# Performance work log

Hardware: AMD Instinct MI355X
Metric: run time of the kernel (lower is better)

Reference implementation:

```python
import jax, jax.numpy as jnp
import numpy as np

N_NODES = 50000
EPS = 1e-7      # GENConv message epsilon
BN_EPS = 1e-5   # BatchNorm1d eps
N_AGGR = 2


def setup_inputs() -> dict:
    key = jax.random.key(0)
    ks = jax.random.split(key, 8)
    C = 64
    E = 800000
    x = jax.random.normal(ks[0], (N_NODES, C), dtype=jnp.float32)
    edge_index = jax.random.randint(ks[1], (2, E), 0, N_NODES, dtype=jnp.int64)
    # per-GENConv MLP params, stacked over the N_AGGR layers
    W1 = jax.random.normal(ks[2], (N_AGGR, C, 2 * C), dtype=jnp.float32) * (1.0 / np.sqrt(C))
    b1 = jnp.zeros((N_AGGR, 2 * C), dtype=jnp.float32)
    gamma = jnp.ones((N_AGGR, 2 * C), dtype=jnp.float32)
    beta = jnp.zeros((N_AGGR, 2 * C), dtype=jnp.float32)
    W2 = jax.random.normal(ks[3], (N_AGGR, 2 * C, C), dtype=jnp.float32) * (1.0 / np.sqrt(2 * C))
    b2 = jnp.zeros((N_AGGR, C), dtype=jnp.float32)
    t = jnp.ones((N_AGGR,), dtype=jnp.float32)  # learnable softmax temperature
    return {"x": x, "edge_index": edge_index, "W1": W1, "b1": b1,
            "gamma": gamma, "beta": beta, "W2": W2, "b2": b2, "t": t}


def _gen_conv(x, src, dst, W1_l, b1_l, gamma_l, beta_l, W2_l, b2_l, t_l):
    # message: relu(x_j) + eps  (edge_attr is None)
    m = jax.nn.relu(x[src]) + EPS                      # [E, C]
    # softmax aggregation over edges grouped by destination node
    logits = m * t_l                                   # [E, C]
    seg_max = jax.ops.segment_max(logits, dst, num_segments=N_NODES)  # [N, C]
    ex = jnp.exp(logits - seg_max[dst])                # [E, C]
    den = jax.ops.segment_sum(ex, dst, num_segments=N_NODES)          # [N, C]
    alpha = ex / (den[dst] + 1e-16)                    # [E, C]
    aggr = jax.ops.segment_sum(m * alpha, dst, num_segments=N_NODES)  # [N, C]
    # residual then MLP: Linear(C,2C) -> BatchNorm1d (train-mode stats) -> ReLU -> Linear(2C,C)
    h = aggr + x
    h = h @ W1_l + b1_l                                # [N, 2C]
    mean = h.mean(axis=0)
    var = h.var(axis=0)                                # biased variance (torch BN)
    h = (h - mean) / jnp.sqrt(var + BN_EPS) * gamma_l + beta_l
    h = jax.nn.relu(h)
    h = h @ W2_l + b2_l                                # [N, C]
    return h


def reference(x, edge_index, W1, b1, gamma, beta, W2, b2, t):
    src = edge_index[0]
    dst = edge_index[1]
    for l in range(N_AGGR):
        x = _gen_conv(x, src, dst, W1[l], b1[l], gamma[l], beta[l], W2[l], b2[l], t[l])
        x = jax.nn.relu(x)
        # dropout in eval mode == identity
    return x
```

## Files before the change

### kernel.cpp

```cpp
#include <hip/hip_runtime.h>
#include <math.h>

#define NN 50000
#define EPSM 1e-7f
#define BN_EPS 1e-5f
#define NBK 391


__global__ __launch_bounds__(256) void bucket_hist_kernel(
    const int* __restrict__ dst, int* __restrict__ bhist, int E,
    unsigned* __restrict__ mm0, float* __restrict__ bn0){
  __shared__ int h[NBK];
  int t = threadIdx.x;
  if (blockIdx.x == 0){
    if (t < 64) mm0[t] = 0x7F7FFFFFu;
    else if (t < 128) mm0[t] = 0u;
    bn0[t] = 0.f;
  }
  for (int i = t; i < NBK; i += 256) h[i] = 0;
  __syncthreads();
  int e0 = blockIdx.x * 4096;
  int cnt = min(4096, E - e0);
  for (int i = t; i < cnt; i += 256) atomicAdd(&h[dst[e0 + i] >> 7], 1);
  __syncthreads();
  for (int i = t; i < NBK; i += 256) if (h[i]) atomicAdd(&bhist[i], h[i]);
}

__global__ void bucket_scan_kernel(const int* __restrict__ bhist,
                                   int* __restrict__ bbase, int* __restrict__ gcur){
  int lane = threadIdx.x;
  int loc[7]; int s = 0;
#pragma unroll
  for (int k = 0; k < 7; ++k){
    int i = lane * 7 + k;
    int v = (i < NBK) ? bhist[i] : 0;
    loc[k] = s; s += v;
  }
  int sc = s;
#pragma unroll
  for (int o = 1; o < 64; o <<= 1){
    int n = __shfl_up(sc, o);
    if (lane >= o) sc += n;
  }
  int exc = sc - s;
#pragma unroll
  for (int k = 0; k < 7; ++k){
    int i = lane * 7 + k;
    if (i < NBK){ bbase[i] = exc + loc[k]; gcur[i] = exc + loc[k]; }
    else if (i == NBK) bbase[i] = exc + loc[k];
  }
}

__global__ __launch_bounds__(256) void bucket_scatter_kernel(
    const int* __restrict__ src, const int* __restrict__ dst,
    int* __restrict__ gcur, unsigned* __restrict__ packed_g, int E){
  __shared__ int hist[NBK], offs[NBK], gb[NBK], curk[NBK];
  __shared__ unsigned stage[4096];
  __shared__ int gpos[4096];
  int t = threadIdx.x;
  for (int i = t; i < NBK; i += 256) hist[i] = 0;
  __syncthreads();
  int e0 = blockIdx.x * 4096;
  int cnt = min(4096, E - e0);
  unsigned pk[16]; int bk[16];
  int nmine = 0;
  for (int i = t; i < cnt; i += 256){
    int d = dst[e0 + i], s = src[e0 + i];
    pk[nmine] = ((unsigned)d << 16) | (unsigned)s;
    bk[nmine] = d >> 7;
    atomicAdd(&hist[bk[nmine]], 1);
    ++nmine;
  }
  __syncthreads();
  if (t < 64){
    int loc[7]; int s = 0;
#pragma unroll
    for (int k = 0; k < 7; ++k){
      int i = t * 7 + k;
      int v = (i < NBK) ? hist[i] : 0;
      loc[k] = s; s += v;
    }
    int sc = s;
#pragma unroll
    for (int o = 1; o < 64; o <<= 1){
      int n = __shfl_up(sc, o);
      if (t >= o) sc += n;
    }
    int exc = sc - s;
#pragma unroll
    for (int k = 0; k < 7; ++k){
      int i = t * 7 + k;
      if (i < NBK) offs[i] = exc + loc[k];
    }
  }
  __syncthreads();
  for (int i = t; i < NBK; i += 256){
    int h = hist[i];
    gb[i] = h ? atomicAdd(&gcur[i], h) : 0;
    curk[i] = offs[i];
  }
  __syncthreads();
  for (int k = 0; k < nmine; ++k){
    int b = bk[k];
    int p = atomicAdd(&curk[b], 1);
    stage[p] = pk[k];
    gpos[p] = gb[b] + (p - offs[b]);
  }
  __syncthreads();
  for (int j = t; j < cnt; j += 256) packed_g[gpos[j]] = stage[j];
}

__global__ __launch_bounds__(256) void bucket_place_kernel(
    const unsigned* __restrict__ packed_g, const int* __restrict__ bbase,
    int* __restrict__ start_g, int* __restrict__ end_g,
    int* __restrict__ srcs_g, int N){
  __shared__ int deg[128], off[128], cur[128];
  __shared__ int sstage[4096];
  int b = blockIdx.x, t = threadIdx.x;
  int beg = bbase[b], cnt = bbase[b + 1] - beg;
  if (t < 128) deg[t] = 0;
  __syncthreads();
  for (int j = t; j < cnt; j += 256)
    atomicAdd(&deg[(packed_g[beg + j] >> 16) & 127], 1);
  __syncthreads();
  if (t < 64){
    int i0 = t * 2;
    int v0 = deg[i0], v1 = deg[i0 + 1];
    int s = v0 + v1;
    int sc = s;
#pragma unroll
    for (int o = 1; o < 64; o <<= 1){
      int n = __shfl_up(sc, o);
      if (t >= o) sc += n;
    }
    int exc = sc - s;
    off[i0] = exc; off[i0 + 1] = exc + v0;
  }
  __syncthreads();
  int node0 = b * 128;
  if (t < 128){
    int node = node0 + t;
    if (node < N){
      start_g[node] = beg + off[t];
      end_g[node] = beg + off[t] + deg[t];
    }
    cur[t] = off[t];
  }
  __syncthreads();
  if (cnt <= 4096){
    for (int j = t; j < cnt; j += 256){
      unsigned p = packed_g[beg + j];
      int lp = atomicAdd(&cur[(p >> 16) & 127], 1);
      sstage[lp] = (int)(p & 0xFFFFu);
    }
    __syncthreads();
    for (int j = t; j < cnt; j += 256) srcs_g[beg + j] = sstage[j];
  } else {
    for (int j = t; j < cnt; j += 256){
      unsigned p = packed_g[beg + j];
      int lp = atomicAdd(&cur[(p >> 16) & 127], 1);
      srcs_g[beg + lp] = (int)(p & 0xFFFFu);
    }
  }
}


__global__ __launch_bounds__(256) void colminmax_kernel(
    const float* __restrict__ x, unsigned* __restrict__ mm,
    unsigned short* __restrict__ mh, int N){
  __shared__ unsigned smn[256], smx[256];
  int c = threadIdx.x & 63;
  int slot = blockIdx.x * 4 + (threadIdx.x >> 6);
  float mx = 0.f, mn = 1e30f;
  for (int r = slot; r < N; r += 256 * 4){
    float m = fmaxf(x[r * 64 + c], 0.f) + EPSM;
    unsigned u = __float_as_uint(m);
    u += 0x7FFFu + ((u >> 16) & 1u);
    unsigned short us = (unsigned short)(u >> 16);
    mh[r * 64 + c] = us;
    float mb = __uint_as_float(((unsigned)us) << 16);
    mx = fmaxf(mx, mb);
    mn = fminf(mn, mb);
  }
  smn[threadIdx.x] = __float_as_uint(mn);
  smx[threadIdx.x] = __float_as_uint(mx);
  __syncthreads();
  if (threadIdx.x < 64){
    unsigned a = smn[c], b = smn[c + 64], d = smn[c + 128], e = smn[c + 192];
    atomicMin(&mm[c], min(min(a, b), min(d, e)));
    a = smx[c]; b = smx[c + 64]; d = smx[c + 128]; e = smx[c + 192];
    atomicMax(&mm[64 + c], max(max(a, b), max(d, e)));
  }
}


__global__ __launch_bounds__(256) void aggregate_kernel(
    const float* __restrict__ x, const unsigned short* __restrict__ mh,
    const int* __restrict__ start, const int* __restrict__ segend,
    const int* __restrict__ srcs, const float* __restrict__ tptr, int layer,
    const unsigned* __restrict__ mm, float* __restrict__ h0, int N){
  int node = blockIdx.x * 4 + (threadIdx.x >> 6);
  if (node >= N) return;
  int c = threadIdx.x & 63;
  float t = tptr[layer];
  float mn = __uint_as_float(mm[c]);
  float mx = __uint_as_float(mm[64 + c]);
  float B = fmaxf(t * mx, t * mn);
  int beg = start[node], end = segend[node];
  float den0 = 0.f, den1 = 0.f, den2 = 0.f, den3 = 0.f;
  float num0 = 0.f, num1 = 0.f, num2 = 0.f, num3 = 0.f;
  int e = beg;
  for (; e + 4 <= end; e += 4){
    int s0 = srcs[e], s1 = srcs[e + 1], s2 = srcs[e + 2], s3 = srcs[e + 3];
    float m0 = __uint_as_float(((unsigned)mh[s0 * 64 + c]) << 16);
    float m1 = __uint_as_float(((unsigned)mh[s1 * 64 + c]) << 16);
    float m2 = __uint_as_float(((unsigned)mh[s2 * 64 + c]) << 16);
    float m3 = __uint_as_float(((unsigned)mh[s3 * 64 + c]) << 16);
    float e0 = __expf(m0 * t - B), e1 = __expf(m1 * t - B);
    float e2 = __expf(m2 * t - B), e3 = __expf(m3 * t - B);
    den0 += e0; num0 += m0 * e0;
    den1 += e1; num1 += m1 * e1;
    den2 += e2; num2 += m2 * e2;
    den3 += e3; num3 += m3 * e3;
  }
  for (; e < end; ++e){
    int s = srcs[e];
    float m = __uint_as_float(((unsigned)mh[s * 64 + c]) << 16);
    float ex = __expf(m * t - B);
    den0 += ex; num0 += m * ex;
  }
  float den = (den0 + den1) + (den2 + den3);
  float num = (num0 + num1) + (num2 + num3);
  h0[node * 64 + c] = num / (den + 1e-16f) + x[node * 64 + c];
}


__global__ __launch_bounds__(256) void gemm1_kernel(
    const float* __restrict__ h0, const float* __restrict__ W1,
    const float* __restrict__ b1, float* __restrict__ h1,
    float* __restrict__ bn, int N,
    unsigned* __restrict__ mm_next, float* __restrict__ bn_next){
  __shared__ float a_lds[64 * 68];
  __shared__ float w_lds[64 * 128];
  int t = threadIdx.x;
  if (mm_next != 0 && blockIdx.x == 0){
    if (t < 64) mm_next[t] = 0x7F7FFFFFu;
    else if (t < 128) mm_next[t] = 0u;
    bn_next[t] = 0.f;
  }
  const float4* wg = (const float4*)W1;
  float4* wl = (float4*)w_lds;
#pragma unroll
  for (int i = 0; i < 8; ++i) wl[t + 256 * i] = wg[t + 256 * i];
  int row0 = blockIdx.x * 64;
#pragma unroll
  for (int i = 0; i < 4; ++i){
    int li = t + 256 * i;
    int r = li >> 4, q = li & 15;
    int gr = row0 + r;
    float4 v = make_float4(0.f, 0.f, 0.f, 0.f);
    if (gr < N) v = ((const float4*)h0)[gr * 16 + q];
    *(float4*)&a_lds[r * 68 + q * 4] = v;
  }
  __syncthreads();
  int tc = t & 31, tr = t >> 5;
  float4 bias = ((const float4*)b1)[tc];
  float acc[8][4];
#pragma unroll
  for (int r = 0; r < 8; ++r){
    acc[r][0] = bias.x; acc[r][1] = bias.y; acc[r][2] = bias.z; acc[r][3] = bias.w;
  }
  for (int k = 0; k < 64; k += 4){
    float4 w0 = *(const float4*)&w_lds[(k + 0) * 128 + tc * 4];
    float4 w1 = *(const float4*)&w_lds[(k + 1) * 128 + tc * 4];
    float4 w2 = *(const float4*)&w_lds[(k + 2) * 128 + tc * 4];
    float4 w3 = *(const float4*)&w_lds[(k + 3) * 128 + tc * 4];
#pragma unroll
    for (int r = 0; r < 8; ++r){
      float4 a = *(const float4*)&a_lds[(tr * 8 + r) * 68 + k];
      acc[r][0] += a.x * w0.x + a.y * w1.x + a.z * w2.x + a.w * w3.x;
      acc[r][1] += a.x * w0.y + a.y * w1.y + a.z * w2.y + a.w * w3.y;
      acc[r][2] += a.x * w0.z + a.y * w1.z + a.z * w2.z + a.w * w3.z;
      acc[r][3] += a.x * w0.w + a.y * w1.w + a.z * w2.w + a.w * w3.w;
    }
  }
  float s[4] = {0.f, 0.f, 0.f, 0.f}, s2[4] = {0.f, 0.f, 0.f, 0.f};
#pragma unroll
  for (int r = 0; r < 8; ++r){
    int gr = row0 + tr * 8 + r;
    if (gr < N){
      *(float4*)&h1[gr * 128 + tc * 4] =
          make_float4(acc[r][0], acc[r][1], acc[r][2], acc[r][3]);
#pragma unroll
      for (int j = 0; j < 4; ++j){ s[j] += acc[r][j]; s2[j] += acc[r][j] * acc[r][j]; }
    }
  }
  __syncthreads();
  float* red = a_lds;
  if (t < 256){ red[t] = 0.f; }
  __syncthreads();
#pragma unroll
  for (int j = 0; j < 4; ++j){
    atomicAdd(&red[tc * 4 + j], s[j]);
    atomicAdd(&red[128 + tc * 4 + j], s2[j]);
  }
  __syncthreads();
  if (t < 256) atomicAdd(&bn[t], red[t]);
}

__global__ __launch_bounds__(256) void gemm2_kernel(
    const float* __restrict__ h1, const float* __restrict__ bn,
    const float* __restrict__ gamma, const float* __restrict__ beta, int layer,
    const float* __restrict__ W2, const float* __restrict__ b2,
    float* __restrict__ xout, int N,
    unsigned* __restrict__ mm_next, unsigned short* __restrict__ mh_next){
  __shared__ float a_lds[64 * 132];
  __shared__ float w_lds[128 * 68];
  __shared__ float ss[256];
  __shared__ unsigned smn[64], smx[64];
  int t = threadIdx.x;
  if (t < 128){
    float mean = bn[t] * (1.f / (float)N);
    float var = bn[128 + t] * (1.f / (float)N) - mean * mean;
    var = fmaxf(var, 0.f);
    float sc = gamma[layer * 128 + t] / sqrtf(var + BN_EPS);
    ss[t] = sc;
    ss[128 + t] = beta[layer * 128 + t] - mean * sc;
  }
  if (t < 64){ smn[t] = 0x7F7FFFFFu; smx[t] = 0u; }
  const float4* wg = (const float4*)W2;
#pragma unroll
  for (int i = 0; i < 8; ++i){
    int li = t + 256 * i;
    int k = li >> 4, q = li & 15;
    *(float4*)&w_lds[k * 68 + q * 4] = wg[li];
  }
  __syncthreads();
  int row0 = blockIdx.x * 64;
#pragma unroll
  for (int i = 0; i < 8; ++i){
    int li = t + 256 * i;
    int r = li >> 5, q = li & 31;
    int gr = row0 + r;
    float4 v = make_float4(0.f, 0.f, 0.f, 0.f);
    if (gr < N) v = ((const float4*)h1)[gr * 32 + q];
    float4 sc = *(const float4*)&ss[q * 4];
    float4 sh = *(const float4*)&ss[128 + q * 4];
    v.x = fmaxf(v.x * sc.x + sh.x, 0.f);
    v.y = fmaxf(v.y * sc.y + sh.y, 0.f);
    v.z = fmaxf(v.z * sc.z + sh.z, 0.f);
    v.w = fmaxf(v.w * sc.w + sh.w, 0.f);
    *(float4*)&a_lds[r * 132 + q * 4] = v;
  }
  __syncthreads();
  int tc = t & 15, tr = t >> 4;
  float4 bias = ((const float4*)b2)[tc];
  float acc[4][4];
#pragma unroll
  for (int r = 0; r < 4; ++r){
    acc[r][0] = bias.x; acc[r][1] = bias.y; acc[r][2] = bias.z; acc[r][3] = bias.w;
  }
  for (int k = 0; k < 128; k += 4){
    float4 w0 = *(const float4*)&w_lds[(k + 0) * 68 + tc * 4];
    float4 w1 = *(const float4*)&w_lds[(k + 1) * 68 + tc * 4];
    float4 w2 = *(const float4*)&w_lds[(k + 2) * 68 + tc * 4];
    float4 w3 = *(const float4*)&w_lds[(k + 3) * 68 + tc * 4];
#pragma unroll
    for (int r = 0; r < 4; ++r){
      float4 a = *(const float4*)&a_lds[(tr * 4 + r) * 132 + k];
      acc[r][0] += a.x * w0.x + a.y * w1.x + a.z * w2.x + a.w * w3.x;
      acc[r][1] += a.x * w0.y + a.y * w1.y + a.z * w2.y + a.w * w3.y;
      acc[r][2] += a.x * w0.z + a.y * w1.z + a.z * w2.z + a.w * w3.z;
      acc[r][3] += a.x * w0.w + a.y * w1.w + a.z * w2.w + a.w * w3.w;
    }
  }
  unsigned mnv[4] = {0x7F7FFFFFu, 0x7F7FFFFFu, 0x7F7FFFFFu, 0x7F7FFFFFu};
  unsigned mxv[4] = {0u, 0u, 0u, 0u};
#pragma unroll
  for (int r = 0; r < 4; ++r){
    int gr = row0 + tr * 4 + r;
    if (gr < N){
      float o0 = fmaxf(acc[r][0], 0.f), o1 = fmaxf(acc[r][1], 0.f);
      float o2 = fmaxf(acc[r][2], 0.f), o3 = fmaxf(acc[r][3], 0.f);
      *(float4*)&xout[gr * 64 + tc * 4] = make_float4(o0, o1, o2, o3);
      if (mh_next != 0){
        unsigned us[4];
        float ov[4] = {o0, o1, o2, o3};
#pragma unroll
        for (int j = 0; j < 4; ++j){
          unsigned u = __float_as_uint(ov[j] + EPSM);
          u += 0x7FFFu + ((u >> 16) & 1u);
          us[j] = u >> 16;
          unsigned fb = us[j] << 16;
          mnv[j] = min(mnv[j], fb);
          mxv[j] = max(mxv[j], fb);
        }
        ((uint2*)mh_next)[gr * 16 + tc] =
            make_uint2(us[0] | (us[1] << 16), us[2] | (us[3] << 16));
      }
    }
  }
  if (mh_next != 0){
    __syncthreads();
#pragma unroll
    for (int j = 0; j < 4; ++j){
      atomicMin(&smn[tc * 4 + j], mnv[j]);
      atomicMax(&smx[tc * 4 + j], mxv[j]);
    }
    __syncthreads();
    if (t < 64){
      atomicMin(&mm_next[t], smn[t]);
      atomicMax(&mm_next[64 + t], smx[t]);
    }
  }
}

extern "C" void kernel_launch(void* const* d_in, const int* in_sizes, int n_in,
                              void* d_out, int out_size, void* d_ws, size_t ws_size,
                              hipStream_t stream) {
  const float* x0    = (const float*)d_in[0];
  const int*   ei    = (const int*)d_in[1];
  const float* W1    = (const float*)d_in[2];
  const float* b1    = (const float*)d_in[3];
  const float* gamma = (const float*)d_in[4];
  const float* beta  = (const float*)d_in[5];
  const float* W2    = (const float*)d_in[6];
  const float* b2    = (const float*)d_in[7];
  const float* tptr  = (const float*)d_in[8];

  const int N = NN;
  const int E = in_sizes[1] / 2;
  const int* src = ei;
  const int* dst = ei + E;

  float* ws  = (float*)d_ws;
  float* h0  = ws;
  float* h1  = h0 + N * 64;
  float* bn0 = h1 + N * 128;
  float* bn1 = bn0 + 256;
  unsigned* mm0 = (unsigned*)(bn1 + 256);
  unsigned* mm1 = mm0 + 128;
  unsigned short* mh = (unsigned short*)(mm1 + 128);
  int* bhist = (int*)(mh + N * 64);
  int* bbase = bhist + NBK;
  int* gcur  = bbase + NBK + 1;
  int* start = gcur + NBK;
  int* segend = start + N;
  unsigned* packed = (unsigned*)(segend + N);
  int* srcs  = (int*)(packed + E);

  float* out = (float*)d_out;

  const int row_blocks = (N + 63) / 64;
  const int chunk_blocks = (E + 4095) / 4096;

  hipMemsetAsync(bhist, 0, NBK * sizeof(int), stream);
  bucket_hist_kernel<<<chunk_blocks, 256, 0, stream>>>(dst, bhist, E, mm0, bn0);
  bucket_scan_kernel<<<1, 64, 0, stream>>>(bhist, bbase, gcur);
  bucket_scatter_kernel<<<chunk_blocks, 256, 0, stream>>>(src, dst, gcur, packed, E);
  bucket_place_kernel<<<NBK, 256, 0, stream>>>(packed, bbase, start, segend, srcs, N);

  colminmax_kernel<<<256, 256, 0, stream>>>(x0, mm0, mh, N);
  aggregate_kernel<<<(N + 3) / 4, 256, 0, stream>>>(x0, mh, start, segend, srcs,
                                                    tptr, 0, mm0, h0, N);
  gemm1_kernel<<<row_blocks, 256, 0, stream>>>(h0, W1, b1, h1, bn0, N, mm1, bn1);
  gemm2_kernel<<<row_blocks, 256, 0, stream>>>(h1, bn0, gamma, beta, 0, W2, b2,
                                               out, N, mm1, mh);
  aggregate_kernel<<<(N + 3) / 4, 256, 0, stream>>>(out, mh, start, segend, srcs,
                                                    tptr, 1, mm1, h0, N);
  gemm1_kernel<<<row_blocks, 256, 0, stream>>>(h0, W1 + 8192, b1 + 128, h1, bn1, N,
                                               (unsigned*)0, (float*)0);
  gemm2_kernel<<<row_blocks, 256, 0, stream>>>(h1, bn1, gamma, beta, 1, W2 + 8192,
                                               b2 + 64, out, N,
                                               (unsigned*)0, (unsigned short*)0);
}
```

Measured before the change: 341.3 us.

## Split bf16 message table into channel halves and narrow source indices to 16-bit

The bf16 message table is stored as two planes of 32 channels, so each 64-byte row gather hits a single cache line. Aggregation now runs a second grid dimension over the channel halves, with each wave splitting a node's edges across two 32-lane slots and combining them with a cross-half shuffle. Source indices are stored as 16-bit values to halve index traffic. The aim is a smaller gather footprint per edge and better L2 locality, at the cost of twice as many blocks, each reading edge indices redundantly, and 16-bit indices silently truncate node ids above 65535 (N=50000 fits).

New measurement: 363.6 us. 6.5% more time.

```diff
diff --git a/kernel.cpp b/kernel.cpp
--- a/kernel.cpp
+++ b/kernel.cpp
@@ -113,7 +113,7 @@
 __global__ __launch_bounds__(256) void bucket_place_kernel(
     const unsigned* __restrict__ packed_g, const int* __restrict__ bbase,
     int* __restrict__ start_g, int* __restrict__ end_g,
-    int* __restrict__ srcs_g, int N){
+    unsigned short* __restrict__ srcs_g, int N){
   __shared__ int deg[128], off[128], cur[128];
   __shared__ int sstage[4096];
   int b = blockIdx.x, t = threadIdx.x;
@@ -154,12 +154,13 @@
       sstage[lp] = (int)(p & 0xFFFFu);
     }
     __syncthreads();
-    for (int j = t; j < cnt; j += 256) srcs_g[beg + j] = sstage[j];
+    for (int j = t; j < cnt; j += 256)
+      srcs_g[beg + j] = (unsigned short)sstage[j];
   } else {
     for (int j = t; j < cnt; j += 256){
       unsigned p = packed_g[beg + j];
       int lp = atomicAdd(&cur[(p >> 16) & 127], 1);
-      srcs_g[beg + lp] = (int)(p & 0xFFFFu);
+      srcs_g[beg + lp] = (unsigned short)(p & 0xFFFFu);
     }
   }
 }
@@ -170,6 +171,8 @@
     unsigned short* __restrict__ mh, int N){
   __shared__ unsigned smn[256], smx[256];
   int c = threadIdx.x & 63;
+  int half = c >> 5, cc = c & 31;
+  unsigned short* mhh = mh + (size_t)half * N * 32;
   int slot = blockIdx.x * 4 + (threadIdx.x >> 6);
   float mx = 0.f, mn = 1e30f;
   for (int r = slot; r < N; r += 256 * 4){
@@ -177,7 +180,7 @@
     unsigned u = __float_as_uint(m);
     u += 0x7FFFu + ((u >> 16) & 1u);
     unsigned short us = (unsigned short)(u >> 16);
-    mh[r * 64 + c] = us;
+    mhh[r * 32 + cc] = us;
     float mb = __uint_as_float(((unsigned)us) << 16);
     mx = fmaxf(mx, mb);
     mn = fminf(mn, mb);
@@ -197,25 +200,29 @@
 __global__ __launch_bounds__(256) void aggregate_kernel(
     const float* __restrict__ x, const unsigned short* __restrict__ mh,
     const int* __restrict__ start, const int* __restrict__ segend,
-    const int* __restrict__ srcs, const float* __restrict__ tptr, int layer,
-    const unsigned* __restrict__ mm, float* __restrict__ h0, int N){
+    const unsigned short* __restrict__ srcs, const float* __restrict__ tptr,
+    int layer, const unsigned* __restrict__ mm, float* __restrict__ h0, int N){
   int node = blockIdx.x * 4 + (threadIdx.x >> 6);
   if (node >= N) return;
-  int c = threadIdx.x & 63;
+  int lane = threadIdx.x & 63;
+  int c = lane & 31, slot = lane >> 5;
+  int half = blockIdx.y;
+  int ch = half * 32 + c;
+  const unsigned short* mhh = mh + (size_t)half * N * 32;
   float t = tptr[layer];
-  float mn = __uint_as_float(mm[c]);
-  float mx = __uint_as_float(mm[64 + c]);
+  float mn = __uint_as_float(mm[ch]);
+  float mx = __uint_as_float(mm[64 + ch]);
   float B = fmaxf(t * mx, t * mn);
   int beg = start[node], end = segend[node];
   float den0 = 0.f, den1 = 0.f, den2 = 0.f, den3 = 0.f;
   float num0 = 0.f, num1 = 0.f, num2 = 0.f, num3 = 0.f;
-  int e = beg;
-  for (; e + 4 <= end; e += 4){
-    int s0 = srcs[e], s1 = srcs[e + 1], s2 = srcs[e + 2], s3 = srcs[e + 3];
-    float m0 = __uint_as_float(((unsigned)mh[s0 * 64 + c]) << 16);
-    float m1 = __uint_as_float(((unsigned)mh[s1 * 64 + c]) << 16);
-    float m2 = __uint_as_float(((unsigned)mh[s2 * 64 + c]) << 16);
-    float m3 = __uint_as_float(((unsigned)mh[s3 * 64 + c]) << 16);
+  int e = beg + slot;
+  for (; e + 6 < end; e += 8){
+    int s0 = srcs[e], s1 = srcs[e + 2], s2 = srcs[e + 4], s3 = srcs[e + 6];
+    float m0 = __uint_as_float(((unsigned)mhh[s0 * 32 + c]) << 16);
+    float m1 = __uint_as_float(((unsigned)mhh[s1 * 32 + c]) << 16);
+    float m2 = __uint_as_float(((unsigned)mhh[s2 * 32 + c]) << 16);
+    float m3 = __uint_as_float(((unsigned)mhh[s3 * 32 + c]) << 16);
     float e0 = __expf(m0 * t - B), e1 = __expf(m1 * t - B);
     float e2 = __expf(m2 * t - B), e3 = __expf(m3 * t - B);
     den0 += e0; num0 += m0 * e0;
@@ -223,15 +230,18 @@
     den2 += e2; num2 += m2 * e2;
     den3 += e3; num3 += m3 * e3;
   }
-  for (; e < end; ++e){
+  for (; e < end; e += 2){
     int s = srcs[e];
-    float m = __uint_as_float(((unsigned)mh[s * 64 + c]) << 16);
+    float m = __uint_as_float(((unsigned)mhh[s * 32 + c]) << 16);
     float ex = __expf(m * t - B);
     den0 += ex; num0 += m * ex;
   }
   float den = (den0 + den1) + (den2 + den3);
   float num = (num0 + num1) + (num2 + num3);
-  h0[node * 64 + c] = num / (den + 1e-16f) + x[node * 64 + c];
+  den += __shfl_xor(den, 32);
+  num += __shfl_xor(num, 32);
+  if (slot == 0)
+    h0[node * 64 + ch] = num / (den + 1e-16f) + x[node * 64 + ch];
 }
 
 
@@ -395,7 +405,8 @@
           mnv[j] = min(mnv[j], fb);
           mxv[j] = max(mxv[j], fb);
         }
-        ((uint2*)mh_next)[gr * 16 + tc] =
+        unsigned short* mh_half = mh_next + (size_t)(tc >> 3) * N * 32;
+        ((uint2*)mh_half)[gr * 8 + (tc & 7)] =
             make_uint2(us[0] | (us[1] << 16), us[2] | (us[3] << 16));
       }
     }
@@ -447,12 +458,13 @@
   int* start = gcur + NBK;
   int* segend = start + N;
   unsigned* packed = (unsigned*)(segend + N);
-  int* srcs  = (int*)(packed + E);
+  unsigned short* srcs = (unsigned short*)(packed + E);
 
   float* out = (float*)d_out;
 
   const int row_blocks = (N + 63) / 64;
   const int chunk_blocks = (E + 4095) / 4096;
+  const dim3 agg_grid((N + 3) / 4, 2);
 
   hipMemsetAsync(bhist, 0, NBK * sizeof(int), stream);
   bucket_hist_kernel<<<chunk_blocks, 256, 0, stream>>>(dst, bhist, E, mm0, bn0);
@@ -461,13 +473,13 @@
   bucket_place_kernel<<<NBK, 256, 0, stream>>>(packed, bbase, start, segend, srcs, N);
 
   colminmax_kernel<<<256, 256, 0, stream>>>(x0, mm0, mh, N);
-  aggregate_kernel<<<(N + 3) / 4, 256, 0, stream>>>(x0, mh, start, segend, srcs,
-                                                    tptr, 0, mm0, h0, N);
+  aggregate_kernel<<<agg_grid, 256, 0, stream>>>(x0, mh, start, segend, srcs,
+                                                 tptr, 0, mm0, h0, N);
   gemm1_kernel<<<row_blocks, 256, 0, stream>>>(h0, W1, b1, h1, bn0, N, mm1, bn1);
   gemm2_kernel<<<row_blocks, 256, 0, stream>>>(h1, bn0, gamma, beta, 0, W2, b2,
                                                out, N, mm1, mh);
-  aggregate_kernel<<<(N + 3) / 4, 256, 0, stream>>>(out, mh, start, segend, srcs,
-                                                    tptr, 1, mm1, h0, N);
+  aggregate_kernel<<<agg_grid, 256, 0, stream>>>(out, mh, start, segend, srcs,
+                                                 tptr, 1, mm1, h0, N);
   gemm1_kernel<<<row_blocks, 256, 0, stream>>>(h0, W1 + 8192, b1 + 128, h1, bn1, N,
                                                (unsigned*)0, (float*)0);
   gemm2_kernel<<<row_blocks, 256, 0, stream>>>(h1, bn1, gamma, beta, 1, W2 + 8192,
```
